# Performance work log

Measured on AMD Instinct MI355X. Metric: run time of the kernel, lower is better.

Reference implementation:

```python
import jax, jax.numpy as jnp
import numpy as np

N_SRC = 50000
N_DST = 50000
E = 800000
D = 64


def setup_inputs() -> dict:
    key = jax.random.key(0)
    k1, k2, k3, k4 = jax.random.split(key, 4)
    src_emb = jax.random.normal(k1, (N_SRC, D), dtype=jnp.float32)
    e_att = jax.random.uniform(k2, (E, 1), dtype=jnp.float32)
    src_idx = jax.random.randint(k3, (E,), 0, N_SRC, dtype=jnp.int64)
    dst_idx = jax.random.randint(k4, (E,), 0, N_DST, dtype=jnp.int64)
    return {"src_emb": src_emb, "e_att": e_att, "src_idx": src_idx, "dst_idx": dst_idx}


def reference(src_emb, e_att, src_idx, dst_idx):
    # DGL: fn.src_mul_edge('emb_o','att','msg') then fn.sum('msg','emb_n')
    # msg[e] = src_emb[src_idx[e]] * e_att[e]  -> scatter-sum into dst nodes
    msg = src_emb[src_idx] * e_att                      # [E, D]
    emb_n = jax.ops.segment_sum(msg, dst_idx, num_segments=N_DST)  # [N_DST, D]
    return emb_n
```

## Files before the change

### kernel.cpp

```cpp
#include <hip/hip_runtime.h>
#include <hip/hip_fp16.h>


#define D 64
#define CAP 64
#define OVF_CAP 65536
#define NPART 8

__global__ void __launch_bounds__(256)
convert_emb_kernel(const float* __restrict__ src, __half* __restrict__ dst, int n4,
                   int* __restrict__ cursor, int ncur) {
    int i = blockIdx.x * blockDim.x + threadIdx.x;
    if (i < ncur) cursor[i] = 0;
    if (i >= n4) return;
    float4 v = ((const float4*)src)[i];
    ushort4 h;
    h.x = __half_as_ushort(__float2half(v.x));
    h.y = __half_as_ushort(__float2half(v.y));
    h.z = __half_as_ushort(__float2half(v.z));
    h.w = __half_as_ushort(__float2half(v.w));
    ((ushort4*)dst)[i] = h;
}

__global__ void __launch_bounds__(256)
scatter_xcd_kernel(const int* __restrict__ dst_idx, const int* __restrict__ src_idx,
                   const float* __restrict__ e_att, int* __restrict__ cursor,
                   unsigned* __restrict__ payload,
                   int* __restrict__ ovf_count, int* __restrict__ ovf_list,
                   int E, int n_dst, int rpx, int epb4) {
    int x     = blockIdx.x & (NPART - 1);
    int chunk = blockIdx.x >> 3;
    int lo = x * rpx;
    int hi = min(lo + rpx, n_dst);

    int E4 = E >> 2;
    int i0 = chunk * epb4;
    int i1 = min(i0 + epb4, E4);

    for (int i = i0 + threadIdx.x; i < i1; i += 256) {
        int4   d4 = ((const int4*)dst_idx)[i];
        int4   s4 = ((const int4*)src_idx)[i];
        float4 a4 = ((const float4*)e_att)[i];
        int   dd[4] = {d4.x, d4.y, d4.z, d4.w};
        int   ss[4] = {s4.x, s4.y, s4.z, s4.w};
        float aa[4] = {a4.x, a4.y, a4.z, a4.w};
#pragma unroll
        for (int k = 0; k < 4; ++k) {
            int d = dd[k];
            if (d < lo || d >= hi) continue;
            int p = atomicAdd(&cursor[d], 1);
            unsigned pay = (unsigned)ss[k] |
                           ((unsigned)__half_as_ushort(__float2half(aa[k])) << 16);
            if (p < CAP) {
                payload[(size_t)d * CAP + p] = pay;
            } else {
                int oi = atomicAdd(ovf_count, 1);
                if (oi < OVF_CAP) ovf_list[oi] = 4 * i + k;
            }
        }
    }
    if (chunk == 0) {
        for (int e = (E4 << 2) + threadIdx.x; e < E; e += 256) {
            int d = dst_idx[e];
            if (d < lo || d >= hi) continue;
            int p = atomicAdd(&cursor[d], 1);
            unsigned pay = (unsigned)src_idx[e] |
                           ((unsigned)__half_as_ushort(__float2half(e_att[e])) << 16);
            if (p < CAP) payload[(size_t)d * CAP + p] = pay;
            else { int oi = atomicAdd(ovf_count, 1); if (oi < OVF_CAP) ovf_list[oi] = e; }
        }
    }
}

__global__ void __launch_bounds__(256)
gather2_kernel(const __half* __restrict__ emb_h,
               const unsigned* __restrict__ payload,
               const int* __restrict__ cursor,
               const int* __restrict__ dst_idx, const int* __restrict__ src_idx,
               const float* __restrict__ e_att, const float* __restrict__ src_emb,
               const int* __restrict__ ovf_count, const int* __restrict__ ovf_list,
               float* __restrict__ out, int n_dst, int n_src, int rpx) {
    int x    = blockIdx.x & (NPART - 1);
    int g    = blockIdx.x >> 3;
    int wv   = threadIdx.x >> 6;
    int lane = threadIdx.x & 63;
    int sub  = lane >> 5;
    int l31  = lane & 31;

    int local = (g * 4 + wv) * 2 + sub;
    int w = x * rpx + local;
    bool rowvalid = (local < rpx) && (w < n_dst);

    int cn = rowvalid ? cursor[w] : 0;
    int cnt = min(cn, CAP);

    uint2 pp = make_uint2(0u, 0u);
    if (rowvalid) pp = ((const uint2*)(payload + (size_t)w * CAP))[l31];

    int cmax = max(cnt, __shfl_xor(cnt, 32));

    float2 acc = make_float2(0.f, 0.f);
    unsigned smax = (unsigned)(n_src - 1);
    for (int j = 0; j < cmax; j += 4) {
        int sl = (sub << 5) | (j >> 1);
        unsigned pv0 = (unsigned)__shfl((int)pp.x, sl);
        unsigned pv1 = (unsigned)__shfl((int)pp.y, sl);
        unsigned pv2 = (unsigned)__shfl((int)pp.x, sl + 1);
        unsigned pv3 = (unsigned)__shfl((int)pp.y, sl + 1);
        float a0 = (j     < cnt) ? __half2float(__ushort_as_half((unsigned short)(pv0 >> 16))) : 0.f;
        float a1 = (j + 1 < cnt) ? __half2float(__ushort_as_half((unsigned short)(pv1 >> 16))) : 0.f;
        float a2 = (j + 2 < cnt) ? __half2float(__ushort_as_half((unsigned short)(pv2 >> 16))) : 0.f;
        float a3 = (j + 3 < cnt) ? __half2float(__ushort_as_half((unsigned short)(pv3 >> 16))) : 0.f;
        unsigned s0 = min(pv0 & 0xffffu, smax);
        unsigned s1 = min(pv1 & 0xffffu, smax);
        unsigned s2 = min(pv2 & 0xffffu, smax);
        unsigned s3 = min(pv3 & 0xffffu, smax);
        __half2 h0 = ((const __half2*)(emb_h + (size_t)s0 * D))[l31];
        __half2 h1 = ((const __half2*)(emb_h + (size_t)s1 * D))[l31];
        __half2 h2 = ((const __half2*)(emb_h + (size_t)s2 * D))[l31];
        __half2 h3 = ((const __half2*)(emb_h + (size_t)s3 * D))[l31];
        acc.x = fmaf(__low2float(h0),  a0, acc.x);
        acc.y = fmaf(__high2float(h0), a0, acc.y);
        acc.x = fmaf(__low2float(h1),  a1, acc.x);
        acc.y = fmaf(__high2float(h1), a1, acc.y);
        acc.x = fmaf(__low2float(h2),  a2, acc.x);
        acc.y = fmaf(__high2float(h2), a2, acc.y);
        acc.x = fmaf(__low2float(h3),  a3, acc.x);
        acc.y = fmaf(__high2float(h3), a3, acc.y);
    }

    if (rowvalid) {
        if (cn > CAP) {
            int oc = *ovf_count;
            if (oc > OVF_CAP) oc = OVF_CAP;
            for (int i = 0; i < oc; ++i) {
                int e = ovf_list[i];
                if (dst_idx[e] == w) {
                    float a = e_att[e];
                    int   s = src_idx[e];
                    acc.x = fmaf(src_emb[(size_t)s * D + 2 * l31],     a, acc.x);
                    acc.y = fmaf(src_emb[(size_t)s * D + 2 * l31 + 1], a, acc.y);
                }
            }
        }
        ((float2*)(out + (size_t)w * D))[l31] = acc;
    }
}

__global__ void __launch_bounds__(256)
atomic_fallback_kernel(const float* __restrict__ src_emb, const float* __restrict__ e_att,
                       const int* __restrict__ src_idx, const int* __restrict__ dst_idx,
                       float* __restrict__ out, int E) {
    int tid  = blockIdx.x * blockDim.x + threadIdx.x;
    int e    = tid >> 4;
    int part = tid & 15;
    if (e >= E) return;
    int   s = src_idx[e];
    int   d = dst_idx[e];
    float a = e_att[e];
    float4 v = ((const float4*)src_emb)[(size_t)s * 16 + part];
    float* orow = out + (size_t)d * D + part * 4;
    atomicAdd(orow + 0, v.x * a);
    atomicAdd(orow + 1, v.y * a);
    atomicAdd(orow + 2, v.z * a);
    atomicAdd(orow + 3, v.w * a);
}

extern "C" void kernel_launch(void* const* d_in, const int* in_sizes, int n_in,
                              void* d_out, int out_size, void* d_ws, size_t ws_size,
                              hipStream_t stream) {
    const float* src_emb = (const float*)d_in[0];
    const float* e_att   = (const float*)d_in[1];
    const int*   src_idx = (const int*)d_in[2];
    const int*   dst_idx = (const int*)d_in[3];
    float*       out     = (float*)d_out;

    const int E     = in_sizes[2];
    const int n_dst = out_size / D;
    const int n_src = in_sizes[0] / D;

    size_t off_emb = 0;
    size_t off_pay = off_emb + (size_t)n_src * D / 2;
    size_t off_cur = off_pay + (size_t)n_dst * CAP;
    size_t need_ints = off_cur + (size_t)n_dst + 1 + OVF_CAP;

    if (n_src <= 65536 && ws_size >= need_ints * sizeof(int)) {
        __half*   emb_h   = (__half*)d_ws;
        unsigned* payload = (unsigned*)d_ws + off_pay;
        int*      cursor  = (int*)d_ws + off_cur;
        int*      ovf_count = cursor + n_dst;
        int*      ovf_list  = ovf_count + 1;

        const int n4 = n_src * D / 4;
        convert_emb_kernel<<<(n4 + 255) / 256, 256, 0, stream>>>(
            src_emb, emb_h, n4, cursor, n_dst + 1);

        const int rpx = (n_dst + NPART - 1) / NPART;
        const int chunks = 512;
        const int E4 = E >> 2;
        const int epb4 = (E4 + chunks - 1) / chunks;
        scatter_xcd_kernel<<<chunks * NPART, 256, 0, stream>>>(
            dst_idx, src_idx, e_att, cursor, payload, ovf_count, ovf_list,
            E, n_dst, rpx, epb4);

        const int gpb = (rpx + 7) / 8;
        gather2_kernel<<<gpb * NPART, 256, 0, stream>>>(
            emb_h, payload, cursor, dst_idx, src_idx, e_att, src_emb,
            ovf_count, ovf_list, out, n_dst, n_src, rpx);
        return;
    }

    hipMemsetAsync(d_out, 0, (size_t)out_size * sizeof(float), stream);
    atomic_fallback_kernel<<<(E * 16 + 255) / 256, 256, 0, stream>>>(
        src_emb, e_att, src_idx, dst_idx, out, E);
}
```

Before: 131.1 us.

## Fuse fp16 embedding conversion into scatter kernel and streamline gather payload loads

Merges the fp32-to-fp16 embedding conversion into the scatter launch as extra blocks and zeroes the cursor array with a memset, so one kernel launch goes away and the conversion can overlap with the scatter. The scatter now tests the four destination indices first and skips loading src_idx and e_att when none belong to this partition. The gather reads one payload word per lane for the first 32 edges and handles the rest in a serial tail loop, trading the wider vector load for lower register pressure and a slower path on high-degree rows. The conversion blocks share the grid with scatter work, so emb_h must be finished before the gather launch, which stream order guarantees.

```diff
diff --git a/kernel.cpp b/kernel.cpp
--- a/kernel.cpp
+++ b/kernel.cpp
@@ -8,46 +8,53 @@
 #define NPART 8
 
 __global__ void __launch_bounds__(256)
-convert_emb_kernel(const float* __restrict__ src, __half* __restrict__ dst, int n4,
-                   int* __restrict__ cursor, int ncur) {
-    int i = blockIdx.x * blockDim.x + threadIdx.x;
-    if (i < ncur) cursor[i] = 0;
-    if (i >= n4) return;
-    float4 v = ((const float4*)src)[i];
-    ushort4 h;
-    h.x = __half_as_ushort(__float2half(v.x));
-    h.y = __half_as_ushort(__float2half(v.y));
-    h.z = __half_as_ushort(__float2half(v.z));
-    h.w = __half_as_ushort(__float2half(v.w));
-    ((ushort4*)dst)[i] = h;
-}
-
-__global__ void __launch_bounds__(256)
-scatter_xcd_kernel(const int* __restrict__ dst_idx, const int* __restrict__ src_idx,
-                   const float* __restrict__ e_att, int* __restrict__ cursor,
-                   unsigned* __restrict__ payload,
-                   int* __restrict__ ovf_count, int* __restrict__ ovf_list,
-                   int E, int n_dst, int rpx, int epb4) {
+scatter_conv_kernel(const int* __restrict__ dst_idx, const int* __restrict__ src_idx,
+                    const float* __restrict__ e_att, int* __restrict__ cursor,
+                    unsigned* __restrict__ payload,
+                    int* __restrict__ ovf_count, int* __restrict__ ovf_list,
+                    const float* __restrict__ src_emb, __half* __restrict__ emb_h,
+                    int E, int n_dst, int rpx, int epb4, int SB, int n4) {
+    if ((int)blockIdx.x >= SB) {
+        int i = ((int)blockIdx.x - SB) * 256 + threadIdx.x;
+        if (i < n4) {
+            float4 v = ((const float4*)src_emb)[i];
+            ushort4 h;
+            h.x = __half_as_ushort(__float2half(v.x));
+            h.y = __half_as_ushort(__float2half(v.y));
+            h.z = __half_as_ushort(__float2half(v.z));
+            h.w = __half_as_ushort(__float2half(v.w));
+            ((ushort4*)emb_h)[i] = h;
+        }
+        return;
+    }
+
     int x     = blockIdx.x & (NPART - 1);
     int chunk = blockIdx.x >> 3;
-    int lo = x * rpx;
-    int hi = min(lo + rpx, n_dst);
+    int lo  = x * rpx;
+    int hi  = min(lo + rpx, n_dst);
+    unsigned span = (unsigned)(hi - lo);
 
     int E4 = E >> 2;
     int i0 = chunk * epb4;
     int i1 = min(i0 + epb4, E4);
 
     for (int i = i0 + threadIdx.x; i < i1; i += 256) {
-        int4   d4 = ((const int4*)dst_idx)[i];
+        int4 d4 = ((const int4*)dst_idx)[i];
+        bool m0 = (unsigned)(d4.x - lo) < span;
+        bool m1 = (unsigned)(d4.y - lo) < span;
+        bool m2 = (unsigned)(d4.z - lo) < span;
+        bool m3 = (unsigned)(d4.w - lo) < span;
+        if (!(m0 | m1 | m2 | m3)) continue;
         int4   s4 = ((const int4*)src_idx)[i];
         float4 a4 = ((const float4*)e_att)[i];
         int   dd[4] = {d4.x, d4.y, d4.z, d4.w};
         int   ss[4] = {s4.x, s4.y, s4.z, s4.w};
         float aa[4] = {a4.x, a4.y, a4.z, a4.w};
+        bool  mm[4] = {m0, m1, m2, m3};
 #pragma unroll
         for (int k = 0; k < 4; ++k) {
+            if (!mm[k]) continue;
             int d = dd[k];
-            if (d < lo || d >= hi) continue;
             int p = atomicAdd(&cursor[d], 1);
             unsigned pay = (unsigned)ss[k] |
                            ((unsigned)__half_as_ushort(__float2half(aa[k])) << 16);
@@ -62,7 +69,7 @@
     if (chunk == 0) {
         for (int e = (E4 << 2) + threadIdx.x; e < E; e += 256) {
             int d = dst_idx[e];
-            if (d < lo || d >= hi) continue;
+            if ((unsigned)(d - lo) >= span) continue;
             int p = atomicAdd(&cursor[d], 1);
             unsigned pay = (unsigned)src_idx[e] |
                            ((unsigned)__half_as_ushort(__float2half(e_att[e])) << 16);
@@ -91,26 +98,27 @@
     int w = x * rpx + local;
     bool rowvalid = (local < rpx) && (w < n_dst);
 
-    int cn = rowvalid ? cursor[w] : 0;
+    int cn  = rowvalid ? cursor[w] : 0;
     int cnt = min(cn, CAP);
-
-    uint2 pp = make_uint2(0u, 0u);
-    if (rowvalid) pp = ((const uint2*)(payload + (size_t)w * CAP))[l31];
-
-    int cmax = max(cnt, __shfl_xor(cnt, 32));
+    int c32 = min(cnt, 32);
+
+    unsigned pp = 0u;
+    if (rowvalid) pp = payload[(size_t)w * CAP + l31];
+
+    int cmax = max(c32, __shfl_xor(c32, 32));
 
     float2 acc = make_float2(0.f, 0.f);
     unsigned smax = (unsigned)(n_src - 1);
     for (int j = 0; j < cmax; j += 4) {
-        int sl = (sub << 5) | (j >> 1);
-        unsigned pv0 = (unsigned)__shfl((int)pp.x, sl);
-        unsigned pv1 = (unsigned)__shfl((int)pp.y, sl);
-        unsigned pv2 = (unsigned)__shfl((int)pp.x, sl + 1);
-        unsigned pv3 = (unsigned)__shfl((int)pp.y, sl + 1);
-        float a0 = (j     < cnt) ? __half2float(__ushort_as_half((unsigned short)(pv0 >> 16))) : 0.f;
-        float a1 = (j + 1 < cnt) ? __half2float(__ushort_as_half((unsigned short)(pv1 >> 16))) : 0.f;
-        float a2 = (j + 2 < cnt) ? __half2float(__ushort_as_half((unsigned short)(pv2 >> 16))) : 0.f;
-        float a3 = (j + 3 < cnt) ? __half2float(__ushort_as_half((unsigned short)(pv3 >> 16))) : 0.f;
+        int sl = (sub << 5) + j;
+        unsigned pv0 = (unsigned)__shfl((int)pp, sl);
+        unsigned pv1 = (unsigned)__shfl((int)pp, sl + 1);
+        unsigned pv2 = (unsigned)__shfl((int)pp, sl + 2);
+        unsigned pv3 = (unsigned)__shfl((int)pp, sl + 3);
+        float a0 = (j     < c32) ? __half2float(__ushort_as_half((unsigned short)(pv0 >> 16))) : 0.f;
+        float a1 = (j + 1 < c32) ? __half2float(__ushort_as_half((unsigned short)(pv1 >> 16))) : 0.f;
+        float a2 = (j + 2 < c32) ? __half2float(__ushort_as_half((unsigned short)(pv2 >> 16))) : 0.f;
+        float a3 = (j + 3 < c32) ? __half2float(__ushort_as_half((unsigned short)(pv3 >> 16))) : 0.f;
         unsigned s0 = min(pv0 & 0xffffu, smax);
         unsigned s1 = min(pv1 & 0xffffu, smax);
         unsigned s2 = min(pv2 & 0xffffu, smax);
@@ -127,6 +135,17 @@
         acc.y = fmaf(__high2float(h2), a2, acc.y);
         acc.x = fmaf(__low2float(h3),  a3, acc.x);
         acc.y = fmaf(__high2float(h3), a3, acc.y);
+    }
+
+    if (rowvalid & (cnt > 32)) {
+        for (int j = 32; j < cnt; ++j) {
+            unsigned pv = payload[(size_t)w * CAP + j];
+            float a = __half2float(__ushort_as_half((unsigned short)(pv >> 16)));
+            unsigned s = min(pv & 0xffffu, smax);
+            __half2 h = ((const __half2*)(emb_h + (size_t)s * D))[l31];
+            acc.x = fmaf(__low2float(h),  a, acc.x);
+            acc.y = fmaf(__high2float(h), a, acc.y);
+        }
     }
 
     if (rowvalid) {
@@ -191,17 +210,19 @@
         int*      ovf_count = cursor + n_dst;
         int*      ovf_list  = ovf_count + 1;
 
-        const int n4 = n_src * D / 4;
-        convert_emb_kernel<<<(n4 + 255) / 256, 256, 0, stream>>>(
-            src_emb, emb_h, n4, cursor, n_dst + 1);
+        hipMemsetAsync(cursor, 0, ((size_t)n_dst + 1) * sizeof(int), stream);
 
         const int rpx = (n_dst + NPART - 1) / NPART;
         const int chunks = 512;
+        const int SB = chunks * NPART;
         const int E4 = E >> 2;
         const int epb4 = (E4 + chunks - 1) / chunks;
-        scatter_xcd_kernel<<<chunks * NPART, 256, 0, stream>>>(
+        const int n4 = n_src * D / 4;
+        const int CB = (n4 + 255) / 256;
+
+        scatter_conv_kernel<<<SB + CB, 256, 0, stream>>>(
             dst_idx, src_idx, e_att, cursor, payload, ovf_count, ovf_list,
-            E, n_dst, rpx, epb4);
+            src_emb, emb_h, E, n_dst, rpx, epb4, SB, n4);
 
         const int gpb = (rpx + 7) / 8;
         gather2_kernel<<<gpb * NPART, 256, 0, stream>>>(
```

New measurement: 130.4 us. About the same (-0.5%).
